# Optimization experiments

Hardware: AMD Instinct MI355X
Metric: run time of the kernel (lower is better)

The kernel has to match this reference:

```python
import jax, jax.numpy as jnp
import numpy as np

G = 2000      # num_genes
TF = 64       # num_tf
B = 32        # batch (cells)
_peaks = 5 + (np.arange(G) % 46)          # ragged peaks per gene, avg ~27
T = int(_peaks.sum())                      # 54736 total peak columns
E = G * 16                                 # directed edges before symmetrization


def setup_inputs() -> dict:
    key = jax.random.key(0)
    ks = jax.random.split(key, 8)
    x = jax.random.normal(ks[0], (B, TF, T), jnp.float32)
    # gene id of each peak column (sorted, ragged segment structure = cut[])
    gene_ids = jnp.asarray(np.repeat(np.arange(G), _peaks), jnp.int32)
    # all per-gene subNet Linear weights flattened into one [TF, T] table
    w_sub = jax.random.normal(ks[1], (TF, T), jnp.float32) * 0.02
    b_sub = jax.random.normal(ks[2], (G,), jnp.float32) * 0.02
    rng = np.random.default_rng(1)
    src = rng.integers(0, G, E)
    dst = rng.integers(0, G, E)
    ei = np.stack([np.concatenate([src, dst]), np.concatenate([dst, src])])
    edge_index = jnp.asarray(ei, jnp.int32)                 # [2, 2E], symmetrized
    w_conv = jax.random.normal(ks[3], (1, 2), jnp.float32) * 0.5   # GCN lin weight (in=1, out=2)
    b_conv = jax.random.normal(ks[4], (2,), jnp.float32) * 0.1
    w_out = jax.random.normal(ks[5], (G * 2, 3), jnp.float32) * 0.02
    b_out = jax.random.normal(ks[6], (3,), jnp.float32) * 0.02
    return dict(x=x, gene_ids=gene_ids, w_sub=w_sub, b_sub=b_sub,
                edge_index=edge_index, w_conv=w_conv, b_conv=b_conv,
                w_out=w_out, b_out=b_out)


def reference(x, gene_ids, w_sub, b_sub, edge_index, w_conv, b_conv, w_out, b_out):
    # --- ragged per-gene subNets: Linear(num_peak_i*TF, 1) each ---
    # out[b,g] = sum_{t, p in gene g} x[b,t,p] * w[g,t,p] + b_sub[g]
    z = (x * w_sub[None]).sum(axis=1)                        # [B, T] reduce over TF
    x_cat = jnp.zeros((x.shape[0], b_sub.shape[0]), x.dtype)
    x_cat = x_cat.at[:, gene_ids].add(z) + b_sub[None]       # segment-sum over peaks
    x_cat = jax.nn.relu(x_cat)                               # cat_activate

    # --- GCNConv(1, 2, add_self_loops=False) on node features [B, G, 1] ---
    h = jnp.einsum('bn,f->bnf', x_cat, w_conv[0])            # lin: [B, G, 2]
    src, dst = edge_index[0], edge_index[1]
    deg = jnp.zeros((b_sub.shape[0],), x.dtype).at[dst].add(1.0)
    dinv = jnp.where(deg > 0, jax.lax.rsqrt(jnp.maximum(deg, 1.0)), 0.0)
    norm = dinv[src] * dinv[dst]                             # [2E]
    msg = h[:, src, :] * norm[None, :, None]                 # gather + scale
    agg = jnp.zeros_like(h).at[:, dst, :].add(msg) + b_conv  # scatter-add + bias
    g = jax.nn.relu(agg).reshape(x.shape[0], -1)             # [B, G*2]

    out = g @ w_out + b_out                                   # [B, 3]
    return x_cat, g, out
```

## Files before the change

kernel.cpp:

```cpp
#include <hip/hip_runtime.h>


__global__ __launch_bounds__(256) void k_subnet4(
        const float* __restrict__ x, const float* __restrict__ w_sub,
        const int* __restrict__ gene_ids, float* __restrict__ acc,
        int TF, int T, int G, int B) {
    int t = (blockIdx.x * blockDim.x + threadIdx.x) * 4;
    if (t >= T) return;
    int b0 = blockIdx.y * 4;
    int nb = B - b0; if (nb > 4) nb = 4;
    const size_t planeT = (size_t)TF * T;

    if (t + 3 < T && (T % 4) == 0) {
        const size_t strideV = (size_t)T / 4;
        const float4* wp  = (const float4*)(w_sub + t);
        const float4* xp0 = (const float4*)(x + (size_t)(b0 + 0) * planeT + t);
        const float4* xp1 = (const float4*)(x + (size_t)(b0 + 1) * planeT + t);
        const float4* xp2 = (const float4*)(x + (size_t)(b0 + 2) * planeT + t);
        const float4* xp3 = (const float4*)(x + (size_t)(b0 + 3) * planeT + t);

        float4 a0 = make_float4(0.f,0.f,0.f,0.f);
        float4 a1 = a0, a2 = a0, a3 = a0;

        if (nb == 4) {
            #pragma unroll 4
            for (int tf = 0; tf < TF; ++tf) {
                size_t off = (size_t)tf * strideV;
                float4 wv = wp[off];
                float4 x0 = xp0[off];
                float4 x1 = xp1[off];
                float4 x2 = xp2[off];
                float4 x3 = xp3[off];
                a0.x += x0.x*wv.x; a0.y += x0.y*wv.y; a0.z += x0.z*wv.z; a0.w += x0.w*wv.w;
                a1.x += x1.x*wv.x; a1.y += x1.y*wv.y; a1.z += x1.z*wv.z; a1.w += x1.w*wv.w;
                a2.x += x2.x*wv.x; a2.y += x2.y*wv.y; a2.z += x2.z*wv.z; a2.w += x2.w*wv.w;
                a3.x += x3.x*wv.x; a3.y += x3.y*wv.y; a3.z += x3.z*wv.z; a3.w += x3.w*wv.w;
            }
        } else {
            for (int tf = 0; tf < TF; ++tf) {
                size_t off = (size_t)tf * strideV;
                float4 wv = wp[off];
                if (nb > 0) { float4 xv = xp0[off]; a0.x += xv.x*wv.x; a0.y += xv.y*wv.y; a0.z += xv.z*wv.z; a0.w += xv.w*wv.w; }
                if (nb > 1) { float4 xv = xp1[off]; a1.x += xv.x*wv.x; a1.y += xv.y*wv.y; a1.z += xv.z*wv.z; a1.w += xv.w*wv.w; }
                if (nb > 2) { float4 xv = xp2[off]; a2.x += xv.x*wv.x; a2.y += xv.y*wv.y; a2.z += xv.z*wv.z; a2.w += xv.w*wv.w; }
            }
        }

        int g0 = gene_ids[t], g1 = gene_ids[t+1], g2 = gene_ids[t+2], g3 = gene_ids[t+3];
        float4 as[4] = {a0, a1, a2, a3};
        for (int bb = 0; bb < nb; ++bb) {
            float* base = acc + (size_t)(b0 + bb) * G;
            float4 a = as[bb];
            float v = a.x; int cg = g0;
            if (g1 == cg) v += a.y; else { atomicAdd(base + cg, v); cg = g1; v = a.y; }
            if (g2 == cg) v += a.z; else { atomicAdd(base + cg, v); cg = g2; v = a.z; }
            if (g3 == cg) v += a.w; else { atomicAdd(base + cg, v); cg = g3; v = a.w; }
            atomicAdd(base + cg, v);
        }
    } else {
        for (int bb = 0; bb < nb; ++bb) {
            int b = b0 + bb;
            for (int tt = t; tt < T && tt < t + 4; ++tt) {
                float a = 0.f;
                for (int tf = 0; tf < TF; ++tf)
                    a += x[(size_t)b * planeT + (size_t)tf * T + tt] * w_sub[(size_t)tf * T + tt];
                atomicAdd(acc + (size_t)b * G + gene_ids[tt], a);
            }
        }
    }
}

__global__ void k_xcat(const float* __restrict__ acc, const float* __restrict__ b_sub,
                       float* __restrict__ xcat, int BG, int G) {
    int i = blockIdx.x * blockDim.x + threadIdx.x;
    if (i >= BG) return;
    int g = i % G;
    float v = acc[i] + b_sub[g];
    xcat[i] = v > 0.f ? v : 0.f;
}

__global__ void k_deg(const int* __restrict__ ei, float* __restrict__ deg, int E2) {
    int e = blockIdx.x * blockDim.x + threadIdx.x;
    if (e < E2) atomicAdd(&deg[ei[E2 + e]], 1.0f);
}

__global__ void k_dinv(float* __restrict__ deg, int G) {
    int g = blockIdx.x * blockDim.x + threadIdx.x;
    if (g < G) {
        float d = deg[g];
        deg[g] = (d > 0.f) ? (1.0f / sqrtf(fmaxf(d, 1.0f))) : 0.f;
    }
}

__global__ void k_norm(const int* __restrict__ ei, const float* __restrict__ dinv,
                       float* __restrict__ norm, int E2) {
    int e = blockIdx.x * blockDim.x + threadIdx.x;
    if (e < E2) norm[e] = dinv[ei[e]] * dinv[ei[E2 + e]];
}

__global__ void k_scatter4(const float* __restrict__ xcat, const int* __restrict__ ei,
                           const float* __restrict__ norm, float* __restrict__ s,
                           int G, int E2, int B) {
    int e = blockIdx.x * blockDim.x + threadIdx.x;
    if (e >= E2) return;
    int b0 = blockIdx.y * 4;
    int nb = B - b0; if (nb > 4) nb = 4;
    int src = ei[e], dst = ei[E2 + e];
    float nm = norm[e];
    for (int bb = 0; bb < nb; ++bb) {
        size_t row = (size_t)(b0 + bb) * G;
        atomicAdd(&s[row + dst], xcat[row + src] * nm);
    }
}

__global__ void k_gout(const float* __restrict__ s, const float* __restrict__ w_conv,
                       const float* __restrict__ b_conv, const float* __restrict__ w_out,
                       const float* __restrict__ b_out, float* __restrict__ gout,
                       float* __restrict__ outfin, int G) {
    int b = blockIdx.x;
    float wc0 = w_conv[0], wc1 = w_conv[1];
    float bc0 = b_conv[0], bc1 = b_conv[1];
    float a0 = 0.f, a1 = 0.f, a2 = 0.f;
    float2* grow = (float2*)(gout + (size_t)b * 2 * G);
    for (int n = threadIdx.x; n < G; n += blockDim.x) {
        float sv = s[(size_t)b * G + n];
        float g0 = fmaxf(sv * wc0 + bc0, 0.f);
        float g1 = fmaxf(sv * wc1 + bc1, 0.f);
        grow[n] = make_float2(g0, g1);
        const float* w0 = w_out + (size_t)(2 * n) * 3;
        a0 += g0 * w0[0] + g1 * w0[3];
        a1 += g0 * w0[1] + g1 * w0[4];
        a2 += g0 * w0[2] + g1 * w0[5];
    }
    __shared__ float red[3][256];
    red[0][threadIdx.x] = a0; red[1][threadIdx.x] = a1; red[2][threadIdx.x] = a2;
    __syncthreads();
    for (int st = blockDim.x / 2; st > 0; st >>= 1) {
        if ((int)threadIdx.x < st) {
            red[0][threadIdx.x] += red[0][threadIdx.x + st];
            red[1][threadIdx.x] += red[1][threadIdx.x + st];
            red[2][threadIdx.x] += red[2][threadIdx.x + st];
        }
        __syncthreads();
    }
    if (threadIdx.x == 0) {
        outfin[b * 3 + 0] = red[0][0] + b_out[0];
        outfin[b * 3 + 1] = red[1][0] + b_out[1];
        outfin[b * 3 + 2] = red[2][0] + b_out[2];
    }
}

extern "C" void kernel_launch(void* const* d_in, const int* in_sizes, int n_in,
                              void* d_out, int out_size, void* d_ws, size_t ws_size,
                              hipStream_t stream) {
    const float* x        = (const float*)d_in[0];
    const int*   gene_ids = (const int*)d_in[1];
    const float* w_sub    = (const float*)d_in[2];
    const float* b_sub    = (const float*)d_in[3];
    const int*   ei       = (const int*)d_in[4];
    const float* w_conv   = (const float*)d_in[5];
    const float* b_conv   = (const float*)d_in[6];
    const float* w_out    = (const float*)d_in[7];
    const float* b_out    = (const float*)d_in[8];

    const int G  = in_sizes[3];
    const int T  = in_sizes[1];
    const int TF = in_sizes[2] / T;
    const int B  = in_sizes[0] / (TF * T);
    const int E2 = in_sizes[4] / 2;
    const int BG = B * G;

    float* acc  = (float*)d_ws;
    float* deg  = acc + BG;
    float* s    = deg + G;
    float* norm = s + BG;
    size_t zero_bytes = (size_t)(BG + G + BG) * sizeof(float);
    hipMemsetAsync(d_ws, 0, zero_bytes, stream);

    float* out_xcat = (float*)d_out;
    float* out_g    = out_xcat + BG;
    float* out_fin  = out_g + (size_t)2 * BG;

    k_deg <<<(E2 + 255) / 256, 256, 0, stream>>>(ei, deg, E2);
    k_dinv<<<(G  + 255) / 256, 256, 0, stream>>>(deg, G);
    k_norm<<<(E2 + 255) / 256, 256, 0, stream>>>(ei, deg, norm, E2);

    {
        int tthreads = (T + 3) / 4;
        dim3 grid((tthreads + 255) / 256, (B + 3) / 4);
        k_subnet4<<<grid, 256, 0, stream>>>(x, w_sub, gene_ids, acc, TF, T, G, B);
    }
    k_xcat<<<(BG + 255) / 256, 256, 0, stream>>>(acc, b_sub, out_xcat, BG, G);
    {
        dim3 grid((E2 + 255) / 256, (B + 3) / 4);
        k_scatter4<<<grid, 256, 0, stream>>>(out_xcat, ei, norm, s, G, E2, B);
    }
    k_gout<<<B, 256, 0, stream>>>(s, w_conv, b_conv, w_out, b_out, out_g, out_fin, G);
}
```

Measured before the change: 785.7 us.

## Fuse GCN tail into one per-batch kernel using shared-memory atomics

Replaces the xcat, degree, dinv, norm, scatter and output kernels with one kernel per batch row. Each block recomputes node degrees and the normalized scatter in shared memory, using LDS atomics instead of global atomics. This removes several launches, the norm buffer and most of the workspace memset. In exchange each of the 32 blocks redundantly walks all 64000 edges serially with 256 threads, so parallelism in the tail is much lower.

```diff
diff --git a/kernel.cpp b/kernel.cpp
--- a/kernel.cpp
+++ b/kernel.cpp
@@ -70,60 +70,51 @@
     }
 }
 
-__global__ void k_xcat(const float* __restrict__ acc, const float* __restrict__ b_sub,
-                       float* __restrict__ xcat, int BG, int G) {
-    int i = blockIdx.x * blockDim.x + threadIdx.x;
-    if (i >= BG) return;
-    int g = i % G;
-    float v = acc[i] + b_sub[g];
-    xcat[i] = v > 0.f ? v : 0.f;
-}
+__global__ __launch_bounds__(256) void k_tail(
+        const float* __restrict__ acc, const float* __restrict__ b_sub,
+        const int* __restrict__ ei,
+        const float* __restrict__ w_conv, const float* __restrict__ b_conv,
+        const float* __restrict__ w_out, const float* __restrict__ b_out,
+        float* __restrict__ out_xcat, float* __restrict__ out_g,
+        float* __restrict__ out_fin, int G, int E2) {
+    extern __shared__ float sh[];
+    float* xc  = sh;
+    float* dg  = sh + G;
+    float* ss  = sh + 2 * G;
+    float* red = sh + 3 * G;
+    const int b = blockIdx.x;
+    const int tid = threadIdx.x, nt = blockDim.x;
 
-__global__ void k_deg(const int* __restrict__ ei, float* __restrict__ deg, int E2) {
-    int e = blockIdx.x * blockDim.x + threadIdx.x;
-    if (e < E2) atomicAdd(&deg[ei[E2 + e]], 1.0f);
-}
+    for (int n = tid; n < G; n += nt) {
+        float v = fmaxf(acc[(size_t)b * G + n] + b_sub[n], 0.f);
+        xc[n] = v;
+        out_xcat[(size_t)b * G + n] = v;
+        dg[n] = 0.f;
+        ss[n] = 0.f;
+    }
+    __syncthreads();
 
-__global__ void k_dinv(float* __restrict__ deg, int G) {
-    int g = blockIdx.x * blockDim.x + threadIdx.x;
-    if (g < G) {
-        float d = deg[g];
-        deg[g] = (d > 0.f) ? (1.0f / sqrtf(fmaxf(d, 1.0f))) : 0.f;
+    for (int e = tid; e < E2; e += nt)
+        atomicAdd(&dg[ei[E2 + e]], 1.0f);
+    __syncthreads();
+    for (int n = tid; n < G; n += nt) {
+        float d = dg[n];
+        dg[n] = (d > 0.f) ? rsqrtf(fmaxf(d, 1.0f)) : 0.f;
     }
-}
+    __syncthreads();
 
-__global__ void k_norm(const int* __restrict__ ei, const float* __restrict__ dinv,
-                       float* __restrict__ norm, int E2) {
-    int e = blockIdx.x * blockDim.x + threadIdx.x;
-    if (e < E2) norm[e] = dinv[ei[e]] * dinv[ei[E2 + e]];
-}
+    for (int e = tid; e < E2; e += nt) {
+        int src = ei[e], dst = ei[E2 + e];
+        atomicAdd(&ss[dst], xc[src] * dg[src] * dg[dst]);
+    }
+    __syncthreads();
 
-__global__ void k_scatter4(const float* __restrict__ xcat, const int* __restrict__ ei,
-                           const float* __restrict__ norm, float* __restrict__ s,
-                           int G, int E2, int B) {
-    int e = blockIdx.x * blockDim.x + threadIdx.x;
-    if (e >= E2) return;
-    int b0 = blockIdx.y * 4;
-    int nb = B - b0; if (nb > 4) nb = 4;
-    int src = ei[e], dst = ei[E2 + e];
-    float nm = norm[e];
-    for (int bb = 0; bb < nb; ++bb) {
-        size_t row = (size_t)(b0 + bb) * G;
-        atomicAdd(&s[row + dst], xcat[row + src] * nm);
-    }
-}
-
-__global__ void k_gout(const float* __restrict__ s, const float* __restrict__ w_conv,
-                       const float* __restrict__ b_conv, const float* __restrict__ w_out,
-                       const float* __restrict__ b_out, float* __restrict__ gout,
-                       float* __restrict__ outfin, int G) {
-    int b = blockIdx.x;
-    float wc0 = w_conv[0], wc1 = w_conv[1];
-    float bc0 = b_conv[0], bc1 = b_conv[1];
+    const float wc0 = w_conv[0], wc1 = w_conv[1];
+    const float bc0 = b_conv[0], bc1 = b_conv[1];
     float a0 = 0.f, a1 = 0.f, a2 = 0.f;
-    float2* grow = (float2*)(gout + (size_t)b * 2 * G);
-    for (int n = threadIdx.x; n < G; n += blockDim.x) {
-        float sv = s[(size_t)b * G + n];
+    float2* grow = (float2*)(out_g + (size_t)b * 2 * G);
+    for (int n = tid; n < G; n += nt) {
+        float sv = ss[n];
         float g0 = fmaxf(sv * wc0 + bc0, 0.f);
         float g1 = fmaxf(sv * wc1 + bc1, 0.f);
         grow[n] = make_float2(g0, g1);
@@ -132,21 +123,20 @@
         a1 += g0 * w0[1] + g1 * w0[4];
         a2 += g0 * w0[2] + g1 * w0[5];
     }
-    __shared__ float red[3][256];
-    red[0][threadIdx.x] = a0; red[1][threadIdx.x] = a1; red[2][threadIdx.x] = a2;
+    red[0 * nt + tid] = a0; red[1 * nt + tid] = a1; red[2 * nt + tid] = a2;
     __syncthreads();
-    for (int st = blockDim.x / 2; st > 0; st >>= 1) {
-        if ((int)threadIdx.x < st) {
-            red[0][threadIdx.x] += red[0][threadIdx.x + st];
-            red[1][threadIdx.x] += red[1][threadIdx.x + st];
-            red[2][threadIdx.x] += red[2][threadIdx.x + st];
+    for (int st = nt / 2; st > 0; st >>= 1) {
+        if (tid < st) {
+            red[0 * nt + tid] += red[0 * nt + tid + st];
+            red[1 * nt + tid] += red[1 * nt + tid + st];
+            red[2 * nt + tid] += red[2 * nt + tid + st];
         }
         __syncthreads();
     }
-    if (threadIdx.x == 0) {
-        outfin[b * 3 + 0] = red[0][0] + b_out[0];
-        outfin[b * 3 + 1] = red[1][0] + b_out[1];
-        outfin[b * 3 + 2] = red[2][0] + b_out[2];
+    if (tid == 0) {
+        out_fin[b * 3 + 0] = red[0 * nt] + b_out[0];
+        out_fin[b * 3 + 1] = red[1 * nt] + b_out[1];
+        out_fin[b * 3 + 2] = red[2 * nt] + b_out[2];
     }
 }
 
@@ -170,30 +160,24 @@
     const int E2 = in_sizes[4] / 2;
     const int BG = B * G;
 
-    float* acc  = (float*)d_ws;
-    float* deg  = acc + BG;
-    float* s    = deg + G;
-    float* norm = s + BG;
-    size_t zero_bytes = (size_t)(BG + G + BG) * sizeof(float);
-    hipMemsetAsync(d_ws, 0, zero_bytes, stream);
+    float* acc = (float*)d_ws;
+    hipMemsetAsync(acc, 0, (size_t)BG * sizeof(float), stream);
 
     float* out_xcat = (float*)d_out;
     float* out_g    = out_xcat + BG;
     float* out_fin  = out_g + (size_t)2 * BG;
-
-    k_deg <<<(E2 + 255) / 256, 256, 0, stream>>>(ei, deg, E2);
-    k_dinv<<<(G  + 255) / 256, 256, 0, stream>>>(deg, G);
-    k_norm<<<(E2 + 255) / 256, 256, 0, stream>>>(ei, deg, norm, E2);
 
     {
         int tthreads = (T + 3) / 4;
         dim3 grid((tthreads + 255) / 256, (B + 3) / 4);
         k_subnet4<<<grid, 256, 0, stream>>>(x, w_sub, gene_ids, acc, TF, T, G, B);
     }
-    k_xcat<<<(BG + 255) / 256, 256, 0, stream>>>(acc, b_sub, out_xcat, BG, G);
+
     {
-        dim3 grid((E2 + 255) / 256, (B + 3) / 4);
-        k_scatter4<<<grid, 256, 0, stream>>>(out_xcat, ei, norm, s, G, E2, B);
+        const int nt = 256;
+        size_t shbytes = ((size_t)3 * G + 3 * nt) * sizeof(float);
+        k_tail<<<B, nt, shbytes, stream>>>(acc, b_sub, ei, w_conv, b_conv,
+                                           w_out, b_out, out_xcat, out_g,
+                                           out_fin, G, E2);
     }
-    k_gout<<<B, 256, 0, stream>>>(s, w_conv, b_conv, w_out, b_out, out_g, out_fin, G);
 }
```

Measured after the change: 826.2 us. 5.2% more time.
